# Optimization experiments

Measured on AMD Instinct MI355X. Metric: run time of the kernel, lower is better.

The kernel has to match this reference:

```python
import jax, jax.numpy as jnp
import numpy as np

N = 16384          # batch
K = 4096           # num_neurons per LogicLayer
L = 4              # num_layers
IN0 = 4            # first layer in_dim (= 2*D from cat([x,-x]))
CLASSES = 2
TAU = 1.0


def setup_inputs() -> dict:
    key = jax.random.key(0)
    k1, k2, k3 = jax.random.split(key, 3)
    rng = np.random.default_rng(0)
    x = jax.random.normal(k1, (N, 2), dtype=jnp.float32)
    w0 = jax.random.normal(k2, (K, 16), dtype=jnp.float32)
    ws = jax.random.normal(k3, (L - 1, K, 16), dtype=jnp.float32)
    ia0 = jnp.asarray(rng.integers(0, IN0, size=(K,)), dtype=jnp.int32)
    ib0 = jnp.asarray(rng.integers(0, IN0, size=(K,)), dtype=jnp.int32)
    ia = jnp.asarray(rng.integers(0, K, size=(L - 1, K)), dtype=jnp.int32)
    ib = jnp.asarray(rng.integers(0, K, size=(L - 1, K)), dtype=jnp.int32)
    return dict(x=x, w0=w0, ws=ws, ia0=ia0, ib0=ib0, ia=ia, ib=ib)


def logic_layer(h, w, idx_a, idx_b):
    """Differentiable logic layer (difflogic, training mode).

    out = sum_i softmax(w)_i * op_i(a, b) over the 16 two-input boolean
    functions. All 16 ops are multilinear in (a, b), so the weighted sum
    collapses exactly to c0 + ca*a + cb*b + cab*a*b with per-neuron coeffs.
    """
    p = jax.nn.softmax(w, axis=-1)  # [k, 16]
    a = h[:, idx_a]                 # [N, k]
    b = h[:, idx_b]                 # [N, k]
    ca = p[:, 2] + p[:, 3] + p[:, 6] + p[:, 7] - p[:, 8] - p[:, 9] - p[:, 12] - p[:, 13]
    cb = p[:, 4] + p[:, 5] + p[:, 6] + p[:, 7] - p[:, 8] - p[:, 9] - p[:, 10] - p[:, 11]
    cab = (p[:, 1] - p[:, 2] - p[:, 4] - 2.0 * p[:, 6] - p[:, 7]
           + p[:, 8] + 2.0 * p[:, 9] + p[:, 11] + p[:, 13] - p[:, 14])
    c0 = p[:, 8] + p[:, 9] + p[:, 10] + p[:, 11] + p[:, 12] + p[:, 13] + p[:, 14] + p[:, 15]
    return c0 + ca * a + cb * b + cab * (a * b)


def _model(iv, w0, ws, ia0, ib0, ia, ib):
    h = logic_layer(iv, w0, ia0, ib0)
    for l in range(ws.shape[0]):  # small fixed layer loop
        h = logic_layer(h, ws[l], ia[l], ib[l])
    # GroupSum(class_count=2, tau=1.0)
    return h.reshape(h.shape[0], CLASSES, -1).sum(-1) / TAU


def reference(x, w0, ws, ia0, ib0, ia, ib):
    mx = jnp.concatenate([x, -x], axis=1)  # [N, 4]
    thresh_space = 0.5

    # ---- ti = 0: thresh = 0, flags all zero -> input_values = tx ----
    tx = (mx > 0.0).astype(jnp.float32)
    iv = tx
    rt0 = _model(iv, w0, ws, ia0, ib0, ia, ib)          # [N, 2]
    # flags[n,d,o] = 1 where input_values[n,d] != results[n,0,o]
    flags = (iv[:, :, None] != rt0[:, None, :]).astype(jnp.float32)  # [N, 4, 2]

    # ---- ti = 1 ----
    lastl = jnp.argmax(rt0, axis=1)                      # [N]
    wadj = jnp.where(lastl > 0, thresh_space, -thresh_space)
    thresh = wadj                                        # started from zeros
    tx = (mx > thresh[:, None]).astype(jnp.float32)
    # nested oi-loop writes tx wherever flags[n,d,oi]==0 for any oi
    upd = jnp.any(flags == 0.0, axis=2)                  # [N, 4]
    iv = jnp.where(upd, tx, iv)
    rt1 = _model(iv, w0, ws, ia0, ib0, ia, ib)           # [N, 2]
    return rt1
```

## Files before the change

### kernel.cpp

```cpp
#include <hip/hip_runtime.h>

#define KN 4096
#define NSAMP 16384
#define NNEUR (4 * KN)

__global__ __launch_bounds__(128) void compute_coeffs(
    const float* __restrict__ w0, const float* __restrict__ wsG,
    float4* __restrict__ coeffs) {
    int g = blockIdx.x * 128 + threadIdx.x;
    const float* wp = (g < KN) ? (w0 + (size_t)g * 16)
                               : (wsG + (size_t)(g - KN) * 16);
    const float4* wr = (const float4*)wp;
    float4 v0 = wr[0], v1 = wr[1], v2 = wr[2], v3 = wr[3];
    float e0 = __expf(v0.x), e1 = __expf(v0.y), e2 = __expf(v0.z), e3 = __expf(v0.w);
    float e4 = __expf(v1.x), e5 = __expf(v1.y), e6 = __expf(v1.z), e7 = __expf(v1.w);
    float e8 = __expf(v2.x), e9 = __expf(v2.y), e10 = __expf(v2.z), e11 = __expf(v2.w);
    float e12 = __expf(v3.x), e13 = __expf(v3.y), e14 = __expf(v3.z), e15 = __expf(v3.w);
    float s = ((e0 + e1) + (e2 + e3)) + ((e4 + e5) + (e6 + e7))
            + ((e8 + e9) + (e10 + e11)) + ((e12 + e13) + (e14 + e15));
    float can  = ((e2 + e3) + (e6 + e7)) - ((e8 + e9) + (e12 + e13));
    float cbn  = ((e4 + e5) + (e6 + e7)) - ((e8 + e9) + (e10 + e11));
    float cabn = (e1 - e2) - (e4 + e7) - 2.0f * e6 + (e8 + e11) + 2.0f * e9
               + (e13 - e14);
    float c0n  = ((e8 + e9) + (e10 + e11)) + ((e12 + e13) + (e14 + e15));
    float inv = 1.0f / s;
    coeffs[g] = make_float4(c0n * inv, can * inv, cbn * inv, cabn * inv);
}

__device__ void eval_network(int pat, const float4* __restrict__ coeffs,
                             const int* __restrict__ ia0, const int* __restrict__ ib0,
                             const int* __restrict__ ia, const int* __restrict__ ib,
                             float* h0, float* h1, float* red, int tid,
                             float& r0, float& r1) {
    #pragma unroll
    for (int i = 0; i < 4; ++i) {
        int k = tid + i * 1024;
        float4 c = coeffs[k];
        float a = (float)((pat >> ia0[k]) & 1);
        float b = (float)((pat >> ib0[k]) & 1);
        h0[k] = c.x + c.y * a + c.z * b + c.w * (a * b);
    }
    __syncthreads();
    #pragma unroll
    for (int l = 0; l < 3; ++l) {
        const int* ial = ia + l * KN;
        const int* ibl = ib + l * KN;
        const float* src = (l & 1) ? h1 : h0;
        float* dst = (l & 1) ? h0 : h1;
        #pragma unroll
        for (int i = 0; i < 4; ++i) {
            int k = tid + i * 1024;
            float4 c = coeffs[(l + 1) * KN + k];
            float a = src[ial[k]];
            float b = src[ibl[k]];
            dst[k] = c.x + c.y * a + c.z * b + c.w * (a * b);
        }
        __syncthreads();
    }
    float s0 = h1[tid] + h1[tid + 1024];
    float s1 = h1[tid + 2048] + h1[tid + 3072];
    #pragma unroll
    for (int off = 32; off > 0; off >>= 1) {
        s0 += __shfl_down(s0, off, 64);
        s1 += __shfl_down(s1, off, 64);
    }
    int wid = tid >> 6, lane = tid & 63;
    if (lane == 0) { red[wid] = s0; red[16 + wid] = s1; }
    __syncthreads();
    if (tid == 0) {
        float t0 = 0.0f, t1 = 0.0f;
        #pragma unroll
        for (int wq = 0; wq < 16; ++wq) { t0 += red[wq]; t1 += red[16 + wq]; }
        red[32] = t0; red[33] = t1;
    }
    __syncthreads();
    r0 = red[32]; r1 = red[33];
}

__global__ __launch_bounds__(1024) void table_scatter(
    const float* __restrict__ x, const float4* __restrict__ coeffs,
    const int* __restrict__ ia0, const int* __restrict__ ib0,
    const int* __restrict__ ia, const int* __restrict__ ib,
    float* __restrict__ out) {
    __shared__ float h0[KN];
    __shared__ float h1[KN];
    __shared__ float red[34];
    __shared__ float tbl[32];
    const int pat = blockIdx.x;
    const int tid = threadIdx.x;

    int a0[4], b0[4], a1[4], b1[4], a2[4], b2[4], a3[4], b3[4];
    float4 cA[4], cB[4];
    #pragma unroll
    for (int i = 0; i < 4; ++i) {
        int k = tid + i * 1024;
        a0[i] = ia0[k];          b0[i] = ib0[k];
        a1[i] = ia[0 * KN + k];  b1[i] = ib[0 * KN + k];
        a2[i] = ia[1 * KN + k];  b2[i] = ib[1 * KN + k];
        a3[i] = ia[2 * KN + k];  b3[i] = ib[2 * KN + k];
        cA[i] = coeffs[k];
        cB[i] = coeffs[KN + k];
    }
    #pragma unroll
    for (int i = 0; i < 4; ++i) {
        int k = tid + i * 1024;
        float a = (float)((pat >> a0[i]) & 1);
        float b = (float)((pat >> b0[i]) & 1);
        h0[k] = cA[i].x + cA[i].y * a + cA[i].z * b + cA[i].w * (a * b);
        cA[i] = coeffs[2 * KN + k];
    }
    __syncthreads();
    #pragma unroll
    for (int i = 0; i < 4; ++i) {
        int k = tid + i * 1024;
        float a = h0[a1[i]], b = h0[b1[i]];
        h1[k] = cB[i].x + cB[i].y * a + cB[i].z * b + cB[i].w * (a * b);
        cB[i] = coeffs[3 * KN + k];
    }
    __syncthreads();
    #pragma unroll
    for (int i = 0; i < 4; ++i) {
        int k = tid + i * 1024;
        float a = h1[a2[i]], b = h1[b2[i]];
        h0[k] = cA[i].x + cA[i].y * a + cA[i].z * b + cA[i].w * (a * b);
    }
    __syncthreads();
    #pragma unroll
    for (int i = 0; i < 4; ++i) {
        int k = tid + i * 1024;
        float a = h0[a3[i]], b = h0[b3[i]];
        h1[k] = cB[i].x + cB[i].y * a + cB[i].z * b + cB[i].w * (a * b);
    }
    __syncthreads();

    float s0 = h1[tid] + h1[tid + 1024];
    float s1 = h1[tid + 2048] + h1[tid + 3072];
    #pragma unroll
    for (int off = 32; off > 0; off >>= 1) {
        s0 += __shfl_down(s0, off, 64);
        s1 += __shfl_down(s1, off, 64);
    }
    int wid = tid >> 6, lane = tid & 63;
    if (lane == 0) { red[wid] = s0; red[16 + wid] = s1; }
    __syncthreads();
    if (tid == 0) {
        float t0 = 0.0f, t1 = 0.0f;
        #pragma unroll
        for (int wq = 0; wq < 16; ++wq) { t0 += red[wq]; t1 += red[16 + wq]; }
        red[32] = t0; red[33] = t1;
    }
    __syncthreads();
    float r0 = red[32], r1 = red[33];

    bool slow = (r0 == 0.0f) || (r0 == 1.0f) || (r1 == 0.0f) || (r1 == 1.0f);
    if (!slow) {
        for (int n = tid; n < NSAMP; n += 1024) {
            float2 xv = ((const float2*)x)[n];
            int p0 = (int)(xv.x > 0.0f) | ((int)(xv.y > 0.0f) << 1)
                   | ((int)(-xv.x > 0.0f) << 2) | ((int)(-xv.y > 0.0f) << 3);
            if (p0 == pat) ((float2*)out)[n] = make_float2(r0, r1);
        }
    } else {
        for (int pp = 0; pp < 16; ++pp) {
            float q0, q1;
            eval_network(pp, coeffs, ia0, ib0, ia, ib, h0, h1, red, tid, q0, q1);
            if (tid == 0) { tbl[2 * pp] = q0; tbl[2 * pp + 1] = q1; }
        }
        __syncthreads();
        for (int n = tid; n < NSAMP; n += 1024) {
            float2 xv = ((const float2*)x)[n];
            float mx[4] = { xv.x, xv.y, -xv.x, -xv.y };
            int p0 = 0;
            float ivf[4];
            #pragma unroll
            for (int i = 0; i < 4; ++i) {
                int b = mx[i] > 0.0f;
                ivf[i] = (float)b;
                p0 |= b << i;
            }
            if (p0 != pat) continue;
            float q0 = tbl[2 * p0], q1 = tbl[2 * p0 + 1];
            int lastl = (q1 > q0) ? 1 : 0;
            float thresh = lastl ? 0.5f : -0.5f;
            int p1 = 0;
            #pragma unroll
            for (int i = 0; i < 4; ++i) {
                bool upd = (ivf[i] == q0) || (ivf[i] == q1);
                int bit = upd ? (int)(mx[i] > thresh) : (int)ivf[i];
                p1 |= bit << i;
            }
            ((float2*)out)[n] = make_float2(tbl[2 * p1], tbl[2 * p1 + 1]);
        }
    }
}

extern "C" void kernel_launch(void* const* d_in, const int* in_sizes, int n_in,
                              void* d_out, int out_size, void* d_ws, size_t ws_size,
                              hipStream_t stream) {
    const float* x   = (const float*)d_in[0];
    const float* w0  = (const float*)d_in[1];
    const float* wsG = (const float*)d_in[2];
    const int* ia0   = (const int*)d_in[3];
    const int* ib0   = (const int*)d_in[4];
    const int* ia    = (const int*)d_in[5];
    const int* ib    = (const int*)d_in[6];

    float4* coeffs = (float4*)d_ws;

    compute_coeffs<<<NNEUR / 128, 128, 0, stream>>>(w0, wsG, coeffs);
    table_scatter<<<16, 1024, 0, stream>>>(x, coeffs, ia0, ib0, ia, ib,
                                           (float*)d_out);
}
```

Before: 19.86 us.

## Pack fp16 coeffs with indices into descriptors and precompute sample patterns

Each neuron's four softmax-derived coefficients are stored as fp16 pairs, together with its two input indices, in one uint4 descriptor. The network pass then needs one vector load per neuron instead of a float4 load plus separate index loads. The prep kernel also computes each sample's 4-bit input pattern into a byte array. The fast scatter path reads 16 patterns per thread with one uint4 load instead of re-reading and re-thresholding x for all samples in every block. The last layer is fused into the group-sum reduction, so it no longer writes to shared memory. The fp16 coefficients reduce precision and may shift the outputs and the exact 0/1 comparison that selects the slow path.

```diff
diff --git a/kernel.cpp b/kernel.cpp
--- a/kernel.cpp
+++ b/kernel.cpp
@@ -1,59 +1,79 @@
 #include <hip/hip_runtime.h>
+#include <hip/hip_fp16.h>
 
 #define KN 4096
 #define NSAMP 16384
-#define NNEUR (4 * KN)
-
-__global__ __launch_bounds__(128) void compute_coeffs(
+
+__global__ __launch_bounds__(256) void prep(
     const float* __restrict__ w0, const float* __restrict__ wsG,
-    float4* __restrict__ coeffs) {
-    int g = blockIdx.x * 128 + threadIdx.x;
-    const float* wp = (g < KN) ? (w0 + (size_t)g * 16)
-                               : (wsG + (size_t)(g - KN) * 16);
-    const float4* wr = (const float4*)wp;
-    float4 v0 = wr[0], v1 = wr[1], v2 = wr[2], v3 = wr[3];
-    float e0 = __expf(v0.x), e1 = __expf(v0.y), e2 = __expf(v0.z), e3 = __expf(v0.w);
-    float e4 = __expf(v1.x), e5 = __expf(v1.y), e6 = __expf(v1.z), e7 = __expf(v1.w);
-    float e8 = __expf(v2.x), e9 = __expf(v2.y), e10 = __expf(v2.z), e11 = __expf(v2.w);
-    float e12 = __expf(v3.x), e13 = __expf(v3.y), e14 = __expf(v3.z), e15 = __expf(v3.w);
-    float s = ((e0 + e1) + (e2 + e3)) + ((e4 + e5) + (e6 + e7))
-            + ((e8 + e9) + (e10 + e11)) + ((e12 + e13) + (e14 + e15));
-    float can  = ((e2 + e3) + (e6 + e7)) - ((e8 + e9) + (e12 + e13));
-    float cbn  = ((e4 + e5) + (e6 + e7)) - ((e8 + e9) + (e10 + e11));
-    float cabn = (e1 - e2) - (e4 + e7) - 2.0f * e6 + (e8 + e11) + 2.0f * e9
-               + (e13 - e14);
-    float c0n  = ((e8 + e9) + (e10 + e11)) + ((e12 + e13) + (e14 + e15));
-    float inv = 1.0f / s;
-    coeffs[g] = make_float4(c0n * inv, can * inv, cbn * inv, cabn * inv);
-}
-
-__device__ void eval_network(int pat, const float4* __restrict__ coeffs,
-                             const int* __restrict__ ia0, const int* __restrict__ ib0,
-                             const int* __restrict__ ia, const int* __restrict__ ib,
-                             float* h0, float* h1, float* red, int tid,
-                             float& r0, float& r1) {
-    #pragma unroll
-    for (int i = 0; i < 4; ++i) {
-        int k = tid + i * 1024;
-        float4 c = coeffs[k];
-        float a = (float)((pat >> ia0[k]) & 1);
-        float b = (float)((pat >> ib0[k]) & 1);
-        h0[k] = c.x + c.y * a + c.z * b + c.w * (a * b);
-    }
-    __syncthreads();
-    #pragma unroll
-    for (int l = 0; l < 3; ++l) {
-        const int* ial = ia + l * KN;
-        const int* ibl = ib + l * KN;
-        const float* src = (l & 1) ? h1 : h0;
-        float* dst = (l & 1) ? h0 : h1;
+    const int* __restrict__ ia0, const int* __restrict__ ib0,
+    const int* __restrict__ ia, const int* __restrict__ ib,
+    const float* __restrict__ x,
+    uint4* __restrict__ desc, unsigned char* __restrict__ pats) {
+    const int bid = blockIdx.x, tid = threadIdx.x;
+    if (bid < 64) {
+        int g = bid * 256 + tid;
+        int layer = g >> 12, k = g & 4095;
+        const float* wp = (layer == 0) ? w0 + (size_t)k * 16
+                                       : wsG + ((size_t)(layer - 1) * KN + k) * 16;
+        const float4* wr = (const float4*)wp;
+        float4 v0 = wr[0], v1 = wr[1], v2 = wr[2], v3 = wr[3];
+        float e0 = __expf(v0.x), e1 = __expf(v0.y), e2 = __expf(v0.z), e3 = __expf(v0.w);
+        float e4 = __expf(v1.x), e5 = __expf(v1.y), e6 = __expf(v1.z), e7 = __expf(v1.w);
+        float e8 = __expf(v2.x), e9 = __expf(v2.y), e10 = __expf(v2.z), e11 = __expf(v2.w);
+        float e12 = __expf(v3.x), e13 = __expf(v3.y), e14 = __expf(v3.z), e15 = __expf(v3.w);
+        float s = ((e0 + e1) + (e2 + e3)) + ((e4 + e5) + (e6 + e7))
+                + ((e8 + e9) + (e10 + e11)) + ((e12 + e13) + (e14 + e15));
+        float can  = ((e2 + e3) + (e6 + e7)) - ((e8 + e9) + (e12 + e13));
+        float cbn  = ((e4 + e5) + (e6 + e7)) - ((e8 + e9) + (e10 + e11));
+        float cabn = (e1 - e2) - (e4 + e7) - 2.0f * e6 + (e8 + e11) + 2.0f * e9
+                   + (e13 - e14);
+        float c0n  = ((e8 + e9) + (e10 + e11)) + ((e12 + e13) + (e14 + e15));
+        float inv = 1.0f / s;
+        int A = (layer == 0) ? ia0[k] : ia[(layer - 1) * KN + k];
+        int B = (layer == 0) ? ib0[k] : ib[(layer - 1) * KN + k];
+        __half2 p01 = __floats2half2_rn(c0n * inv, can * inv);
+        __half2 p23 = __floats2half2_rn(cbn * inv, cabn * inv);
+        uint4 d;
+        d.x = *(unsigned*)&p01;
+        d.y = *(unsigned*)&p23;
+        d.z = (unsigned)A;
+        d.w = (unsigned)B;
+        desc[g] = d;
+    } else {
+        int n = (bid - 64) * 256 + tid;
+        float2 xv = ((const float2*)x)[n];
+        int p0 = (int)(xv.x > 0.0f) | ((int)(xv.y > 0.0f) << 1)
+               | ((int)(-xv.x > 0.0f) << 2) | ((int)(-xv.y > 0.0f) << 3);
+        pats[n] = (unsigned char)p0;
+    }
+}
+
+__device__ __forceinline__ float neuron(uint4 d, float a, float b) {
+    float2 c01 = __half22float2(*(__half2*)&d.x);
+    float2 c23 = __half22float2(*(__half2*)&d.y);
+    return c01.x + c01.y * a + c23.x * b + c23.y * (a * b);
+}
+
+__device__ void eval_desc(int pp, const uint4* __restrict__ desc,
+                          float* h0, float* h1, float* red, int tid,
+                          float& r0, float& r1) {
+    #pragma unroll
+    for (int i = 0; i < 4; ++i) {
+        int k = tid + i * 1024;
+        uint4 d = desc[k];
+        float a = (float)((pp >> d.z) & 1), b = (float)((pp >> d.w) & 1);
+        h0[k] = neuron(d, a, b);
+    }
+    __syncthreads();
+    for (int l = 1; l <= 3; ++l) {
+        const float* src = (l & 1) ? h0 : h1;
+        float* dst = (l & 1) ? h1 : h0;
         #pragma unroll
         for (int i = 0; i < 4; ++i) {
             int k = tid + i * 1024;
-            float4 c = coeffs[(l + 1) * KN + k];
-            float a = src[ial[k]];
-            float b = src[ibl[k]];
-            dst[k] = c.x + c.y * a + c.z * b + c.w * (a * b);
+            uint4 d = desc[l * KN + k];
+            dst[k] = neuron(d, src[d.z], src[d.w]);
         }
         __syncthreads();
     }
@@ -75,13 +95,12 @@
     }
     __syncthreads();
     r0 = red[32]; r1 = red[33];
+    __syncthreads();
 }
 
 __global__ __launch_bounds__(1024) void table_scatter(
-    const float* __restrict__ x, const float4* __restrict__ coeffs,
-    const int* __restrict__ ia0, const int* __restrict__ ib0,
-    const int* __restrict__ ia, const int* __restrict__ ib,
-    float* __restrict__ out) {
+    const uint4* __restrict__ desc, const unsigned char* __restrict__ pats,
+    const float* __restrict__ x, float* __restrict__ out) {
     __shared__ float h0[KN];
     __shared__ float h1[KN];
     __shared__ float red[34];
@@ -89,52 +108,40 @@
     const int pat = blockIdx.x;
     const int tid = threadIdx.x;
 
-    int a0[4], b0[4], a1[4], b1[4], a2[4], b2[4], a3[4], b3[4];
-    float4 cA[4], cB[4];
-    #pragma unroll
-    for (int i = 0; i < 4; ++i) {
-        int k = tid + i * 1024;
-        a0[i] = ia0[k];          b0[i] = ib0[k];
-        a1[i] = ia[0 * KN + k];  b1[i] = ib[0 * KN + k];
-        a2[i] = ia[1 * KN + k];  b2[i] = ib[1 * KN + k];
-        a3[i] = ia[2 * KN + k];  b3[i] = ib[2 * KN + k];
-        cA[i] = coeffs[k];
-        cB[i] = coeffs[KN + k];
-    }
-    #pragma unroll
-    for (int i = 0; i < 4; ++i) {
-        int k = tid + i * 1024;
-        float a = (float)((pat >> a0[i]) & 1);
-        float b = (float)((pat >> b0[i]) & 1);
-        h0[k] = cA[i].x + cA[i].y * a + cA[i].z * b + cA[i].w * (a * b);
-        cA[i] = coeffs[2 * KN + k];
-    }
-    __syncthreads();
-    #pragma unroll
-    for (int i = 0; i < 4; ++i) {
-        int k = tid + i * 1024;
-        float a = h0[a1[i]], b = h0[b1[i]];
-        h1[k] = cB[i].x + cB[i].y * a + cB[i].z * b + cB[i].w * (a * b);
-        cB[i] = coeffs[3 * KN + k];
-    }
-    __syncthreads();
-    #pragma unroll
-    for (int i = 0; i < 4; ++i) {
-        int k = tid + i * 1024;
-        float a = h1[a2[i]], b = h1[b2[i]];
-        h0[k] = cA[i].x + cA[i].y * a + cA[i].z * b + cA[i].w * (a * b);
-    }
-    __syncthreads();
-    #pragma unroll
-    for (int i = 0; i < 4; ++i) {
-        int k = tid + i * 1024;
-        float a = h0[a3[i]], b = h0[b3[i]];
-        h1[k] = cB[i].x + cB[i].y * a + cB[i].z * b + cB[i].w * (a * b);
-    }
-    __syncthreads();
-
-    float s0 = h1[tid] + h1[tid + 1024];
-    float s1 = h1[tid + 2048] + h1[tid + 3072];
+    uint4 dA[4], dB[4];
+    #pragma unroll
+    for (int i = 0; i < 4; ++i) {
+        int k = tid + i * 1024;
+        dA[i] = desc[k];
+        dB[i] = desc[KN + k];
+    }
+    #pragma unroll
+    for (int i = 0; i < 4; ++i) {
+        int k = tid + i * 1024;
+        float a = (float)((pat >> dA[i].z) & 1), b = (float)((pat >> dA[i].w) & 1);
+        h0[k] = neuron(dA[i], a, b);
+        dA[i] = desc[2 * KN + k];
+    }
+    __syncthreads();
+    #pragma unroll
+    for (int i = 0; i < 4; ++i) {
+        int k = tid + i * 1024;
+        h1[k] = neuron(dB[i], h0[dB[i].z], h0[dB[i].w]);
+        dB[i] = desc[3 * KN + k];
+    }
+    __syncthreads();
+    #pragma unroll
+    for (int i = 0; i < 4; ++i) {
+        int k = tid + i * 1024;
+        h0[k] = neuron(dA[i], h1[dA[i].z], h1[dA[i].w]);
+    }
+    __syncthreads();
+    float s0 = 0.0f, s1 = 0.0f;
+    #pragma unroll
+    for (int i = 0; i < 4; ++i) {
+        float o = neuron(dB[i], h0[dB[i].z], h0[dB[i].w]);
+        if (i < 2) s0 += o; else s1 += o;
+    }
     #pragma unroll
     for (int off = 32; off > 0; off >>= 1) {
         s0 += __shfl_down(s0, off, 64);
@@ -154,31 +161,38 @@
 
     bool slow = (r0 == 0.0f) || (r0 == 1.0f) || (r1 == 0.0f) || (r1 == 1.0f);
     if (!slow) {
-        for (int n = tid; n < NSAMP; n += 1024) {
-            float2 xv = ((const float2*)x)[n];
-            int p0 = (int)(xv.x > 0.0f) | ((int)(xv.y > 0.0f) << 1)
-                   | ((int)(-xv.x > 0.0f) << 2) | ((int)(-xv.y > 0.0f) << 3);
-            if (p0 == pat) ((float2*)out)[n] = make_float2(r0, r1);
+        uint4 pv = ((const uint4*)pats)[tid];
+        int base = tid * 16;
+        unsigned wv[4] = { pv.x, pv.y, pv.z, pv.w };
+        #pragma unroll
+        for (int wq = 0; wq < 4; ++wq) {
+            #pragma unroll
+            for (int b = 0; b < 4; ++b) {
+                if (((wv[wq] >> (8 * b)) & 0xffu) == (unsigned)pat) {
+                    int n = base + wq * 4 + b;
+                    ((float2*)out)[n] = make_float2(r0, r1);
+                }
+            }
         }
     } else {
         for (int pp = 0; pp < 16; ++pp) {
             float q0, q1;
-            eval_network(pp, coeffs, ia0, ib0, ia, ib, h0, h1, red, tid, q0, q1);
+            eval_desc(pp, desc, h0, h1, red, tid, q0, q1);
             if (tid == 0) { tbl[2 * pp] = q0; tbl[2 * pp + 1] = q1; }
         }
         __syncthreads();
         for (int n = tid; n < NSAMP; n += 1024) {
+            if (pats[n] != (unsigned char)pat) continue;
             float2 xv = ((const float2*)x)[n];
             float mx[4] = { xv.x, xv.y, -xv.x, -xv.y };
+            float ivf[4];
             int p0 = 0;
-            float ivf[4];
             #pragma unroll
             for (int i = 0; i < 4; ++i) {
                 int b = mx[i] > 0.0f;
                 ivf[i] = (float)b;
                 p0 |= b << i;
             }
-            if (p0 != pat) continue;
             float q0 = tbl[2 * p0], q1 = tbl[2 * p0 + 1];
             int lastl = (q1 > q0) ? 1 : 0;
             float thresh = lastl ? 0.5f : -0.5f;
@@ -205,9 +219,9 @@
     const int* ia    = (const int*)d_in[5];
     const int* ib    = (const int*)d_in[6];
 
-    float4* coeffs = (float4*)d_ws;
-
-    compute_coeffs<<<NNEUR / 128, 128, 0, stream>>>(w0, wsG, coeffs);
-    table_scatter<<<16, 1024, 0, stream>>>(x, coeffs, ia0, ib0, ia, ib,
-                                           (float*)d_out);
-}
+    uint4* desc         = (uint4*)d_ws;
+    unsigned char* pats = (unsigned char*)d_ws + 4 * KN * 16;
+
+    prep<<<128, 256, 0, stream>>>(w0, wsG, ia0, ib0, ia, ib, x, desc, pats);
+    table_scatter<<<16, 1024, 0, stream>>>(desc, pats, x, (float*)d_out);
+}
```

Result: faster. 17.89 us (-9.9%).
